# Performance work log

Hardware: AMD Instinct MI355X
Metric: run time of the kernel (lower is better)

The kernel has to match this reference:

```python
import jax, jax.numpy as jnp
import numpy as np

N = 8192
D = 512            # d_model
E = 8              # num_experts
H = 1024           # expert_hidden_dim
RH = 256           # router_hidden_dim
TOPK = 2
IN_DIM = 9 * D + 3
LN_EPS = 1e-5


def layernorm(x, g, b, eps=LN_EPS):
    m = jnp.mean(x, axis=-1, keepdims=True)
    v = jnp.mean((x - m) ** 2, axis=-1, keepdims=True)
    return (x - m) * jax.lax.rsqrt(v + eps) * g + b


def setup_inputs() -> dict:
    key = jax.random.key(0)
    ks = jax.random.split(key, 16)
    s_in = 1.0 / np.sqrt(IN_DIM)
    s_rh = 1.0 / np.sqrt(RH)
    s_h = 1.0 / np.sqrt(H)
    return {
        "z1": jax.random.normal(ks[0], (N, D), jnp.float32),
        "z2": jax.random.normal(ks[1], (N, D), jnp.float32),
        "z3": jax.random.normal(ks[2], (N, D), jnp.float32),
        "mask": jnp.ones((N, 3), jnp.float32),
        # LayerNorms
        "ln_g": jnp.ones((D,), jnp.float32), "ln_b": jnp.zeros((D,), jnp.float32),
        "lnp_g": jnp.ones((D,), jnp.float32), "lnp_b": jnp.zeros((D,), jnp.float32),
        "oln_g": jnp.ones((D,), jnp.float32), "oln_b": jnp.zeros((D,), jnp.float32),
        # Router MLP
        "r_w1": jax.random.normal(ks[3], (IN_DIM, RH), jnp.float32) * s_in,
        "r_b1": jnp.zeros((RH,), jnp.float32),
        "r_w2": jax.random.normal(ks[4], (RH, E), jnp.float32) * s_rh,
        "r_b2": jnp.zeros((E,), jnp.float32),
        "log_temp": jnp.array(np.log(1.0), jnp.float32),
        # Stacked experts: fc1 [E, IN_DIM, H], fc2 [E, H, D]
        "e_w1": jax.random.normal(ks[5], (E, IN_DIM, H), jnp.float32) * s_in,
        "e_b1": jnp.zeros((E, H), jnp.float32),
        "e_w2": jax.random.normal(ks[6], (E, H, D), jnp.float32) * s_h,
        "e_b2": jnp.zeros((E, D), jnp.float32),
    }


def reference(z1, z2, z3, mask, ln_g, ln_b, lnp_g, lnp_b, oln_g, oln_b,
              r_w1, r_b1, r_w2, r_b2, log_temp, e_w1, e_b1, e_w2, e_b2):
    # --- build fusion input ---
    z1n = layernorm(z1, ln_g, ln_b)
    z2n = layernorm(z2, ln_g, ln_b)
    z3n = layernorm(z3, ln_g, ln_b)
    d12 = layernorm(z1n - z2n, lnp_g, lnp_b)
    d13 = layernorm(z1n - z3n, lnp_g, lnp_b)
    d23 = layernorm(z2n - z3n, lnp_g, lnp_b)
    p12 = layernorm(z1n * z2n, lnp_g, lnp_b)
    p13 = layernorm(z1n * z3n, lnp_g, lnp_b)
    p23 = layernorm(z2n * z3n, lnp_g, lnp_b)
    x = jnp.concatenate([z1n, z2n, z3n, d12, d13, d23, p12, p13, p23, mask], axis=-1)  # [N, 9D+3]

    # --- router: MLP + temperature-scaled top-k softmax ---
    temp = jnp.clip(jnp.exp(log_temp), 1e-3, 100.0)
    rh = jax.nn.gelu(x @ r_w1 + r_b1, approximate=False)
    logits = (rh @ r_w2 + r_b2) / temp                      # [N, E]
    topv, topi = jax.lax.top_k(logits, TOPK)
    keep = jnp.zeros_like(logits).at[jnp.arange(logits.shape[0])[:, None], topi].set(1.0)
    masked_logits = jnp.where(keep == 0, -jnp.inf, logits)
    gate = jax.nn.softmax(masked_logits, axis=-1)           # [N, E]

    # --- dense expert compute (matches torch.stack over experts) ---
    eh = jax.nn.gelu(jnp.einsum('ni,eih->neh', x, e_w1) + e_b1, approximate=False)
    outs = jnp.einsum('neh,ehd->ned', eh, e_w2) + e_b2      # [N, E, D]
    z = jnp.einsum('ne,ned->nd', gate, outs)                # combine

    # --- masked residual ---
    denom = jnp.clip(jnp.sum(mask, axis=1, keepdims=True), 1.0, None)
    z_res = (mask[:, 0:1] * z1n + mask[:, 1:2] * z2n + mask[:, 2:3] * z3n) / denom
    z = z + z_res

    return layernorm(z, oln_g, oln_b)
```

## Files before the change

kernel.cpp:

```cpp
#include <hip/hip_runtime.h>
#include <math.h>

#define N_TOK 8192
#define DMODEL 512
#define NEXP 8
#define HEXP 1024
#define RHDIM 256
#define KP 4672
#define IN_REAL 4611
#define BK 64
#define NPAIR (N_TOK * 2)
#define MAXT 136

typedef unsigned short u16;
typedef __bf16 bf16x8 __attribute__((ext_vector_type(8)));
typedef float f32x4 __attribute__((ext_vector_type(4)));

__device__ inline u16 f2bf(float f) {
    union { float f; unsigned u; } x; x.f = f;
    unsigned r = x.u + 0x7FFFu + ((x.u >> 16) & 1u);
    return (u16)(r >> 16);
}
__device__ inline float bf2f(u16 u) {
    union { unsigned u; float f; } x; x.u = ((unsigned)u) << 16;
    return x.f;
}
__device__ inline float gelu_exact(float v) {
    return 0.5f * v * (1.f + erff(v * 0.70710678118654752440f));
}

__device__ inline void async_cp16(const u16* g, u16* l) {
    __builtin_amdgcn_global_load_lds(
        (const __attribute__((address_space(1))) unsigned int*)g,
        (__attribute__((address_space(3))) unsigned int*)l, 16, 0, 0);
}

template<int M>
__device__ inline void breduce(float (&v)[M], int tid, float* red) {
    #pragma unroll
    for (int o = 32; o > 0; o >>= 1)
        #pragma unroll
        for (int i = 0; i < M; i++) v[i] += __shfl_xor(v[i], o);
    __syncthreads();
    if ((tid & 63) == 0) {
        #pragma unroll
        for (int i = 0; i < M; i++) red[(tid >> 6) * M + i] = v[i];
    }
    __syncthreads();
    if (tid < M) {
        float S = 0.f;
        #pragma unroll
        for (int w8 = 0; w8 < 8; w8++) S += red[w8 * M + tid];
        red[96 + tid] = S;
    }
    __syncthreads();
    #pragma unroll
    for (int i = 0; i < M; i++) v[i] = red[96 + i];
}

__device__ inline float2 bstats512(float v, int tid, float* red) {
    float s = v, q = v * v;
    #pragma unroll
    for (int o = 32; o > 0; o >>= 1) {
        s += __shfl_xor(s, o);
        q += __shfl_xor(q, o);
    }
    __syncthreads();
    if ((tid & 63) == 0) { red[(tid >> 6) * 2] = s; red[(tid >> 6) * 2 + 1] = q; }
    __syncthreads();
    if (tid == 0) {
        float S = 0.f, Q = 0.f;
        #pragma unroll
        for (int i = 0; i < 8; i++) { S += red[i * 2]; Q += red[i * 2 + 1]; }
        float m = S * (1.f / 512.f);
        float var = fmaxf(Q * (1.f / 512.f) - m * m, 0.f);
        red[16] = m;
        red[17] = rsqrtf(var + 1e-5f);
    }
    __syncthreads();
    return make_float2(red[16], red[17]);
}

__global__ __launch_bounds__(256)
void transpose_f32_bf16(const float* __restrict__ src, u16* __restrict__ dhi, u16* __restrict__ dlo,
                        int K0, int KPd, int H, size_t sbatch, size_t dbatch) {
    __shared__ float tile[32][33];
    int bz = blockIdx.z;
    src += (size_t)bz * sbatch;
    size_t dob = (size_t)bz * dbatch;
    int k0 = blockIdx.x * 32, h0 = blockIdx.y * 32;
    int tx = threadIdx.x, ty = threadIdx.y;
    for (int i = ty; i < 32; i += 8) {
        int k = k0 + i;
        tile[i][tx] = (k < K0) ? src[(size_t)k * H + (h0 + tx)] : 0.f;
    }
    __syncthreads();
    for (int i = ty; i < 32; i += 8) {
        int h = h0 + i, k = k0 + tx;
        float v = tile[tx][i];
        u16 hv = f2bf(v);
        dhi[dob + (size_t)h * KPd + k] = hv;
        if (dlo) dlo[dob + (size_t)h * KPd + k] = f2bf(v - bf2f(hv));
    }
}

__global__ __launch_bounds__(512)
void build_x(const float* __restrict__ z1, const float* __restrict__ z2, const float* __restrict__ z3,
             const float* __restrict__ mask,
             const float* __restrict__ ln_g, const float* __restrict__ ln_b,
             const float* __restrict__ lnp_g, const float* __restrict__ lnp_b,
             u16* __restrict__ xhi, u16* __restrict__ xlo) {
    __shared__ float red[108];
    int n = blockIdx.x, d = threadIdx.x;
    float a = z1[(size_t)n * DMODEL + d];
    float b = z2[(size_t)n * DMODEL + d];
    float c = z3[(size_t)n * DMODEL + d];
    float gg = ln_g[d], bb = ln_b[d], pg = lnp_g[d], pb = lnp_b[d];
    size_t base = (size_t)n * KP;

    auto emit = [&](int seg, float v) {
        u16 h = f2bf(v);
        xhi[base + seg * DMODEL + d] = h;
        xlo[base + seg * DMODEL + d] = f2bf(v - bf2f(h));
    };
    auto lnv = [](float v, float s, float q, float g, float bo) {
        float m = s * (1.f / 512.f);
        float var = fmaxf(q * (1.f / 512.f) - m * m, 0.f);
        return (v - m) * rsqrtf(var + 1e-5f) * g + bo;
    };
    float v6[6] = {a, a * a, b, b * b, c, c * c};
    breduce<6>(v6, d, red);
    float z1n = lnv(a, v6[0], v6[1], gg, bb);
    float z2n = lnv(b, v6[2], v6[3], gg, bb);
    float z3n = lnv(c, v6[4], v6[5], gg, bb);
    emit(0, z1n); emit(1, z2n); emit(2, z3n);
    float d12 = z1n - z2n, d13 = z1n - z3n, d23 = z2n - z3n;
    float p12 = z1n * z2n, p13 = z1n * z3n, p23 = z2n * z3n;
    float v12[12] = {d12, d12 * d12, d13, d13 * d13, d23, d23 * d23,
                     p12, p12 * p12, p13, p13 * p13, p23, p23 * p23};
    breduce<12>(v12, d, red);
    emit(3, lnv(d12, v12[0], v12[1], pg, pb));
    emit(4, lnv(d13, v12[2], v12[3], pg, pb));
    emit(5, lnv(d23, v12[4], v12[5], pg, pb));
    emit(6, lnv(p12, v12[6], v12[7], pg, pb));
    emit(7, lnv(p13, v12[8], v12[9], pg, pb));
    emit(8, lnv(p23, v12[10], v12[11], pg, pb));
    if (d < 64) {
        int col = 9 * DMODEL + d;
        float v = (d < 3) ? mask[(size_t)n * 3 + d] : 0.f;
        u16 h = f2bf(v);
        xhi[base + col] = h;
        xlo[base + col] = f2bf(v - bf2f(h));
    }
}

#define GEMM_DEFS4                                                            \
    int t = threadIdx.x;                                                      \
    int lane = t & 63, w = t >> 6;                                            \
    int r8 = lane >> 3;                                                       \
    int ce = ((lane & 7) ^ r8) * 8;         \
    int fr = lane & 15, q4 = lane >> 4;                                       \
    int wm = (w & 1) * 64, wn = (w >> 1) * 64;                                \
    f32x4 acc[4][4];                                                          \
    { f32x4 z4 = {0.f, 0.f, 0.f, 0.f};                                        \
      _Pragma("unroll") for (int i = 0; i < 4; i++)                           \
      _Pragma("unroll") for (int j = 0; j < 4; j++) acc[i][j] = z4; }         \
    u16 *lAp[4], *lBp[4];                                                     \
    _Pragma("unroll") for (int i = 0; i < 4; i++) {                           \
        lAp[i] = lA + (w * 32 + 8 * i) * BK;                                  \
        lBp[i] = lB + (w * 32 + 8 * i) * BK;                                  \
    }

#define GEMM_KSTEP4                                                           \
        __syncthreads();                                                      \
        _Pragma("unroll") for (int i = 0; i < 4; i++) {                       \
            async_cp16(gA[i], lAp[i]); async_cp16(gB[i], lBp[i]);             \
            gA[i] += BK; gB[i] += BK;                                         \
        }                                                                     \
        __syncthreads();                                                      \
        _Pragma("unroll") for (int ks = 0; ks < 2; ks++) {                    \
            bf16x8 af[4], bfr[4];                                             \
            int cofs = (((q4 + ks * 4) ^ (fr & 7)) * 8);                      \
            _Pragma("unroll") for (int i = 0; i < 4; i++)                     \
                af[i] = *(const bf16x8*)&lA[(wm + i * 16 + fr) * BK + cofs];  \
            _Pragma("unroll") for (int j = 0; j < 4; j++)                     \
                bfr[j] = *(const bf16x8*)&lB[(wn + j * 16 + fr) * BK + cofs]; \
            _Pragma("unroll") for (int i = 0; i < 4; i++)                     \
            _Pragma("unroll") for (int j = 0; j < 4; j++)                     \
                acc[i][j] = __builtin_amdgcn_mfma_f32_16x16x32_bf16(af[i], bfr[j], acc[i][j], 0, 0, 0); \
        }

#define GEMM_DEFS8                                                            \
    int t = threadIdx.x;                                                      \
    int lane = t & 63, w = t >> 6;                                            \
    int r8 = lane >> 3;                                                       \
    int ce = ((lane & 7) ^ r8) * 8;         \
    int fr = lane & 15, q4 = lane >> 4;                                       \
    int wm = (w & 1) * 64, wn = (w >> 1) * 64;                                \
    f32x4 acc[4][4];                                                          \
    { f32x4 z4 = {0.f, 0.f, 0.f, 0.f};                                        \
      _Pragma("unroll") for (int i = 0; i < 4; i++)                           \
      _Pragma("unroll") for (int j = 0; j < 4; j++) acc[i][j] = z4; }         \
    u16 *lAp[2], *lBp[4];                                                     \
    _Pragma("unroll") for (int i = 0; i < 2; i++)                             \
        lAp[i] = lA + (w * 16 + 8 * i) * BK;                                  \
    _Pragma("unroll") for (int i = 0; i < 4; i++)                             \
        lBp[i] = lB + (w * 32 + 8 * i) * BK;

#define GEMM_KSTEP8                                                           \
        __syncthreads();                                                      \
        _Pragma("unroll") for (int i = 0; i < 2; i++) {                       \
            async_cp16(gA[i], lAp[i]); gA[i] += BK;                           \
        }                                                                     \
        _Pragma("unroll") for (int i = 0; i < 4; i++) {                       \
            async_cp16(gB[i], lBp[i]); gB[i] += BK;                           \
        }                                                                     \
        __syncthreads();                                                      \
        _Pragma("unroll") for (int ks = 0; ks < 2; ks++) {                    \
            bf16x8 af[4], bfr[4];                                             \
            int cofs = (((q4 + ks * 4) ^ (fr & 7)) * 8);                      \
            _Pragma("unroll") for (int i = 0; i < 4; i++)                     \
                af[i] = *(const bf16x8*)&lA[(wm + i * 16 + fr) * BK + cofs];  \
            _Pragma("unroll") for (int j = 0; j < 4; j++)                     \
                bfr[j] = *(const bf16x8*)&lB[(wn + j * 16 + fr) * BK + cofs]; \
            _Pragma("unroll") for (int i = 0; i < 4; i++)                     \
            _Pragma("unroll") for (int j = 0; j < 4; j++)                     \
                acc[i][j] = __builtin_amdgcn_mfma_f32_16x16x32_bf16(af[i], bfr[j], acc[i][j], 0, 0, 0); \
        }

__global__ __launch_bounds__(512, 4)
void router_fc1(const u16* __restrict__ xhi, const u16* __restrict__ xlo,
                const u16* __restrict__ rw1hi, const u16* __restrict__ rw1lo,
                float* __restrict__ rpart) {
    int mt = blockIdx.x & 63, part = blockIdx.x >> 6;
    int region = part >> 1, half = part & 1;
    const u16* A = (region == 2) ? xlo : xhi;
    const u16* B = (region == 1) ? rw1lo : rw1hi;
    int kbase = half ? 2304 : 0;
    int klen  = half ? 2368 : 2304;

    __shared__ u16 lA[128 * BK];
    __shared__ u16 lB[256 * BK];
    GEMM_DEFS8

    const u16* gA[2]; const u16* gB[4];
    #pragma unroll
    for (int i = 0; i < 2; i++)
        gA[i] = A + (size_t)(mt * 128 + w * 16 + 8 * i + r8) * KP + kbase + ce;
    #pragma unroll
    for (int i = 0; i < 4; i++)
        gB[i] = B + (size_t)(w * 32 + 8 * i + r8) * KP + kbase + ce;

    for (int k0 = 0; k0 < klen; k0 += BK) {
        GEMM_KSTEP8
    }
    float* outp = rpart + (size_t)part * ((size_t)N_TOK * RHDIM);
    int cn = lane & 15;
    #pragma unroll
    for (int i = 0; i < 4; i++)
        #pragma unroll
        for (int rr = 0; rr < 4; rr++) {
            int mg = mt * 128 + wm + i * 16 + q4 * 4 + rr;
            #pragma unroll
            for (int j = 0; j < 4; j++)
                outp[(size_t)mg * RHDIM + wn + j * 16 + cn] = acc[i][j][rr];
        }
}

__global__ __launch_bounds__(256)
void logits_topk(const float* __restrict__ rpart, const float* __restrict__ r_b1,
                 const float* __restrict__ r_w2, const float* __restrict__ r_b2,
                 const float* __restrict__ log_temp,
                 float* __restrict__ pgate, int* __restrict__ pexp,
                 int* __restrict__ lists, int* __restrict__ counts) {
    int t = threadIdx.x, wave = t >> 6, lane = t & 63;
    int n = blockIdx.x * 4 + wave;
    float4 v = {0.f, 0.f, 0.f, 0.f};
    #pragma unroll
    for (int p = 0; p < 6; p++) {
        float4 s = ((const float4*)(rpart + (size_t)p * ((size_t)N_TOK * RHDIM) + (size_t)n * RHDIM))[lane];
        v.x += s.x; v.y += s.y; v.z += s.z; v.w += s.w;
    }
    float4 b1 = ((const float4*)r_b1)[lane];
    float rh0 = gelu_exact(v.x + b1.x);
    float rh1 = gelu_exact(v.y + b1.y);
    float rh2 = gelu_exact(v.z + b1.z);
    float rh3 = gelu_exact(v.w + b1.w);
    int k = lane * 4;
    float p8[8];
    #pragma unroll
    for (int e = 0; e < 8; e++)
        p8[e] = rh0 * r_w2[(k + 0) * 8 + e] + rh1 * r_w2[(k + 1) * 8 + e]
              + rh2 * r_w2[(k + 2) * 8 + e] + rh3 * r_w2[(k + 3) * 8 + e];
    #pragma unroll
    for (int o = 32; o > 0; o >>= 1)
        #pragma unroll
        for (int e = 0; e < 8; e++) p8[e] += __shfl_xor(p8[e], o);
    if (lane == 0) {
        float temp = fminf(fmaxf(expf(log_temp[0]), 1e-3f), 100.f);
        float l[8];
        #pragma unroll
        for (int e = 0; e < 8; e++) l[e] = (p8[e] + r_b2[e]) / temp;
        int i1 = 0;
        #pragma unroll
        for (int i = 1; i < 8; i++) if (l[i] > l[i1]) i1 = i;
        int i2 = (i1 == 0) ? 1 : 0;
        #pragma unroll
        for (int i = 0; i < 8; i++) if (i != i1 && l[i] > l[i2]) i2 = i;
        float p = expf(l[i2] - l[i1]);
        float g1 = 1.f / (1.f + p);
        float g2 = p / (1.f + p);
        pgate[n * 2] = g1;     pexp[n * 2] = i1;
        pgate[n * 2 + 1] = g2; pexp[n * 2 + 1] = i2;
        int pos1 = atomicAdd(&counts[i1], 1);
        lists[(size_t)i1 * N_TOK + pos1] = n * 2;
        int pos2 = atomicAdd(&counts[i2], 1);
        lists[(size_t)i2 * N_TOK + pos2] = n * 2 + 1;
    }
}

__global__ void sched_tiles(const int* __restrict__ counts, int* __restrict__ tiles) {
    if (threadIdx.x == 0) {
        int tcount = 0;
        for (int e = 0; e < NEXP; e++) {
            int nt = (counts[e] + 127) >> 7;
            for (int mt = 0; mt < nt; mt++) tiles[tcount++] = (e << 16) | mt;
        }
        for (; tcount < MAXT; tcount++) tiles[tcount] = -1;
    }
}

__global__ __launch_bounds__(256, 4)
void expert_fc1(const u16* __restrict__ xhi, const u16* __restrict__ w1t,
                const float* __restrict__ e_b1, const int* __restrict__ lists,
                const int* __restrict__ counts, const int* __restrict__ tiles,
                u16* __restrict__ eh) {
    int nt = blockIdx.x & 7, ti = blockIdx.x >> 3;
    int info = tiles[ti];
    if (info < 0) return;
    int e = info >> 16, mt = info & 0xFFFF;
    int cnt = counts[e];

    __shared__ u16 lA[128 * BK];
    __shared__ u16 lB[128 * BK];
    __shared__ int rows[128];
    int tt = threadIdx.x;
    if (tt < 128) {
        int m = mt * 128 + tt;
        rows[tt] = lists[(size_t)e * N_TOK + (m < cnt ? m : 0)];
    }
    __syncthreads();

    GEMM_DEFS4

    const u16* wb = w1t + (size_t)e * HEXP * KP + (size_t)(nt * 128) * KP;
    const u16* gA[4]; const u16* gB[4];
    #pragma unroll
    for (int i = 0; i < 4; i++) {
        gA[i] = xhi + (size_t)(rows[w * 32 + 8 * i + r8] >> 1) * KP + ce;
        gB[i] = wb + (size_t)(w * 32 + 8 * i + r8) * KP + ce;
    }

    for (int k0 = 0; k0 < KP; k0 += BK) {
        GEMM_KSTEP4
    }
    int cn = lane & 15;
    #pragma unroll
    for (int i = 0; i < 4; i++)
        #pragma unroll
        for (int rr = 0; rr < 4; rr++) {
            int ml = wm + i * 16 + q4 * 4 + rr;
            int mg = mt * 128 + ml;
            if (mg < cnt) {
                int entry = rows[ml];
                #pragma unroll
                for (int j = 0; j < 4; j++) {
                    int col = nt * 128 + wn + j * 16 + cn;
                    float v = acc[i][j][rr] + e_b1[(size_t)e * HEXP + col];
                    eh[(size_t)entry * HEXP + col] = f2bf(gelu_exact(v));
                }
            }
        }
}

__global__ __launch_bounds__(512, 4)
void expert_fc2(const u16* __restrict__ eh, const u16* __restrict__ w2t,
                const int* __restrict__ lists, const int* __restrict__ counts,
                const int* __restrict__ tiles, float* __restrict__ outs) {
    int nt = blockIdx.x & 1, ti = blockIdx.x >> 1;
    int info = tiles[ti];
    if (info < 0) return;
    int e = info >> 16, mt = info & 0xFFFF;
    int cnt = counts[e];

    __shared__ u16 lA[128 * BK];
    __shared__ u16 lB[256 * BK];
    __shared__ int rows[128];
    int tt = threadIdx.x;
    if (tt < 128) {
        int m = mt * 128 + tt;
        rows[tt] = lists[(size_t)e * N_TOK + (m < cnt ? m : 0)];
    }
    __syncthreads();

    GEMM_DEFS8

    const u16* wb = w2t + (size_t)e * DMODEL * HEXP + (size_t)(nt * 256) * HEXP;
    const u16* gA[2]; const u16* gB[4];
    #pragma unroll
    for (int i = 0; i < 2; i++)
        gA[i] = eh + (size_t)rows[w * 16 + 8 * i + r8] * HEXP + ce;
    #pragma unroll
    for (int i = 0; i < 4; i++)
        gB[i] = wb + (size_t)(w * 32 + 8 * i + r8) * HEXP + ce;

    for (int k0 = 0; k0 < HEXP; k0 += BK) {
        GEMM_KSTEP8
    }
    int cn = lane & 15;
    #pragma unroll
    for (int i = 0; i < 4; i++)
        #pragma unroll
        for (int rr = 0; rr < 4; rr++) {
            int ml = wm + i * 16 + q4 * 4 + rr;
            int mg = mt * 128 + ml;
            if (mg < cnt) {
                int entry = rows[ml];
                #pragma unroll
                for (int j = 0; j < 4; j++) {
                    int col = nt * 256 + wn + j * 16 + cn;
                    outs[(size_t)entry * DMODEL + col] = acc[i][j][rr];
                }
            }
        }
}

__global__ __launch_bounds__(512)
void combine_ln(const float* __restrict__ outs, const float* __restrict__ pgate,
                const int* __restrict__ pexp, const float* __restrict__ e_b2,
                const float* __restrict__ mask, const u16* __restrict__ xhi,
                const u16* __restrict__ xlo, const float* __restrict__ oln_g,
                const float* __restrict__ oln_b, float* __restrict__ out) {
    __shared__ float red[18];
    int n = blockIdx.x, d = threadIdx.x;
    float g0 = pgate[n * 2], g1 = pgate[n * 2 + 1];
    int e0 = pexp[n * 2], e1 = pexp[n * 2 + 1];
    float o = g0 * (outs[(size_t)(n * 2) * DMODEL + d] + e_b2[(size_t)e0 * DMODEL + d])
            + g1 * (outs[(size_t)(n * 2 + 1) * DMODEL + d] + e_b2[(size_t)e1 * DMODEL + d]);
    float m0 = mask[n * 3 + 0], m1 = mask[n * 3 + 1], m2 = mask[n * 3 + 2];
    float denom = fmaxf(m0 + m1 + m2, 1.f);
    size_t xb = (size_t)n * KP;
    float z1n = bf2f(xhi[xb + d]) + bf2f(xlo[xb + d]);
    float z2n = bf2f(xhi[xb + DMODEL + d]) + bf2f(xlo[xb + DMODEL + d]);
    float z3n = bf2f(xhi[xb + 2 * DMODEL + d]) + bf2f(xlo[xb + 2 * DMODEL + d]);
    float z = o + (m0 * z1n + m1 * z2n + m2 * z3n) / denom;
    float2 st = bstats512(z, d, red);
    out[(size_t)n * DMODEL + d] = (z - st.x) * st.y * oln_g[d] + oln_b[d];
}

extern "C" void kernel_launch(void* const* d_in, const int* in_sizes, int n_in,
                              void* d_out, int out_size, void* d_ws, size_t ws_size,
                              hipStream_t stream) {
    (void)in_sizes; (void)n_in; (void)out_size; (void)ws_size;
    const float* z1       = (const float*)d_in[0];
    const float* z2       = (const float*)d_in[1];
    const float* z3       = (const float*)d_in[2];
    const float* mask     = (const float*)d_in[3];
    const float* ln_g     = (const float*)d_in[4];
    const float* ln_b     = (const float*)d_in[5];
    const float* lnp_g    = (const float*)d_in[6];
    const float* lnp_b    = (const float*)d_in[7];
    const float* oln_g    = (const float*)d_in[8];
    const float* oln_b    = (const float*)d_in[9];
    const float* r_w1     = (const float*)d_in[10];
    const float* r_b1     = (const float*)d_in[11];
    const float* r_w2     = (const float*)d_in[12];
    const float* r_b2     = (const float*)d_in[13];
    const float* log_temp = (const float*)d_in[14];
    const float* e_w1     = (const float*)d_in[15];
    const float* e_b1     = (const float*)d_in[16];
    const float* e_w2     = (const float*)d_in[17];
    const float* e_b2     = (const float*)d_in[18];
    float* out = (float*)d_out;

    char* p = (char*)d_ws;
    auto carve = [&](size_t bytes) { char* r = p; p += (bytes + 255) & ~(size_t)255; return r; };
    u16*   xhi    = (u16*)carve((size_t)N_TOK * KP * 2);
    u16*   xlo    = (u16*)carve((size_t)N_TOK * KP * 2);
    u16*   w1t    = (u16*)carve((size_t)NEXP * HEXP * KP * 2);
    u16*   w2t    = (u16*)carve((size_t)NEXP * DMODEL * HEXP * 2);
    u16*   rw1hi  = (u16*)carve((size_t)RHDIM * KP * 2);
    u16*   rw1lo  = (u16*)carve((size_t)RHDIM * KP * 2);
    float* rpart  = (float*)carve((size_t)6 * N_TOK * RHDIM * 4);
    u16*   eh     = (u16*)carve((size_t)NPAIR * HEXP * 2);
    float* outsb  = (float*)carve((size_t)NPAIR * DMODEL * 4);
    float* pgate  = (float*)carve((size_t)NPAIR * 4);
    int*   pexp   = (int*)carve((size_t)NPAIR * 4);
    int*   lists  = (int*)carve((size_t)NEXP * N_TOK * 4);
    int*   counts = (int*)carve(256);
    int*   tiles  = (int*)carve(MAXT * 4);

    dim3 tb(32, 8);
    transpose_f32_bf16<<<dim3(KP / 32, HEXP / 32, NEXP), tb, 0, stream>>>(
        e_w1, w1t, (u16*)nullptr, IN_REAL, KP, HEXP, (size_t)IN_REAL * HEXP, (size_t)HEXP * KP);
    transpose_f32_bf16<<<dim3(HEXP / 32, DMODEL / 32, NEXP), tb, 0, stream>>>(
        e_w2, w2t, (u16*)nullptr, HEXP, HEXP, DMODEL, (size_t)HEXP * DMODEL, (size_t)DMODEL * HEXP);
    transpose_f32_bf16<<<dim3(KP / 32, RHDIM / 32, 1), tb, 0, stream>>>(
        r_w1, rw1hi, rw1lo, IN_REAL, KP, RHDIM, (size_t)0, (size_t)0);

    build_x<<<N_TOK, 512, 0, stream>>>(z1, z2, z3, mask, ln_g, ln_b, lnp_g, lnp_b, xhi, xlo);

    router_fc1<<<384, 512, 0, stream>>>(xhi, xlo, rw1hi, rw1lo, rpart);

    hipMemsetAsync(counts, 0, 256, stream);
    logits_topk<<<N_TOK / 4, 256, 0, stream>>>(rpart, r_b1, r_w2, r_b2, log_temp,
                                               pgate, pexp, lists, counts);
    sched_tiles<<<1, 64, 0, stream>>>(counts, tiles);

    expert_fc1<<<MAXT * 8, 256, 0, stream>>>(xhi, w1t, e_b1, lists, counts, tiles, eh);
    expert_fc2<<<MAXT * 2, 512, 0, stream>>>(eh, w2t, lists, counts, tiles, outsb);

    combine_ln<<<N_TOK, 512, 0, stream>>>(outsb, pgate, pexp, e_b2, mask, xhi, xlo, oln_g, oln_b, out);
}
```

Measured before the change: 978.0 us.

## Vectorize elementwise kernels, shrink block sizes, and split router hi*hi K range

build_x and combine_ln now use 128 threads per token, with each thread handling 4 elements through float4/ushort4 loads and stores. The block reduction is simplified to two wavefronts. The transpose kernel writes 4-wide packed bf16 stores. router_fc1 splits the dominant hi*hi product into four K chunks, giving 512 blocks and 8 partial buffers, to raise parallelism at the cost of more partial-sum traffic in logits_topk.

```diff
diff --git a/kernel.cpp b/kernel.cpp
--- a/kernel.cpp
+++ b/kernel.cpp
@@ -11,6 +11,7 @@
 #define BK 64
 #define NPAIR (N_TOK * 2)
 #define MAXT 136
+#define NRPART 8
 
 typedef unsigned short u16;
 typedef __bf16 bf16x8 __attribute__((ext_vector_type(8)));
@@ -36,49 +37,19 @@
 }
 
 template<int M>
-__device__ inline void breduce(float (&v)[M], int tid, float* red) {
+__device__ inline void bred128(float (&v)[M], int t, float* red) {
     #pragma unroll
     for (int o = 32; o > 0; o >>= 1)
         #pragma unroll
         for (int i = 0; i < M; i++) v[i] += __shfl_xor(v[i], o);
     __syncthreads();
-    if ((tid & 63) == 0) {
-        #pragma unroll
-        for (int i = 0; i < M; i++) red[(tid >> 6) * M + i] = v[i];
+    if ((t & 63) == 0) {
+        #pragma unroll
+        for (int i = 0; i < M; i++) red[(t >> 6) * M + i] = v[i];
     }
     __syncthreads();
-    if (tid < M) {
-        float S = 0.f;
-        #pragma unroll
-        for (int w8 = 0; w8 < 8; w8++) S += red[w8 * M + tid];
-        red[96 + tid] = S;
-    }
-    __syncthreads();
-    #pragma unroll
-    for (int i = 0; i < M; i++) v[i] = red[96 + i];
-}
-
-__device__ inline float2 bstats512(float v, int tid, float* red) {
-    float s = v, q = v * v;
-    #pragma unroll
-    for (int o = 32; o > 0; o >>= 1) {
-        s += __shfl_xor(s, o);
-        q += __shfl_xor(q, o);
-    }
-    __syncthreads();
-    if ((tid & 63) == 0) { red[(tid >> 6) * 2] = s; red[(tid >> 6) * 2 + 1] = q; }
-    __syncthreads();
-    if (tid == 0) {
-        float S = 0.f, Q = 0.f;
-        #pragma unroll
-        for (int i = 0; i < 8; i++) { S += red[i * 2]; Q += red[i * 2 + 1]; }
-        float m = S * (1.f / 512.f);
-        float var = fmaxf(Q * (1.f / 512.f) - m * m, 0.f);
-        red[16] = m;
-        red[17] = rsqrtf(var + 1e-5f);
-    }
-    __syncthreads();
-    return make_float2(red[16], red[17]);
+    #pragma unroll
+    for (int i = 0; i < M; i++) v[i] = red[i] + red[M + i];
 }
 
 __global__ __launch_bounds__(256)
@@ -95,62 +66,110 @@
         tile[i][tx] = (k < K0) ? src[(size_t)k * H + (h0 + tx)] : 0.f;
     }
     __syncthreads();
-    for (int i = ty; i < 32; i += 8) {
-        int h = h0 + i, k = k0 + tx;
-        float v = tile[tx][i];
-        u16 hv = f2bf(v);
-        dhi[dob + (size_t)h * KPd + k] = hv;
-        if (dlo) dlo[dob + (size_t)h * KPd + k] = f2bf(v - bf2f(hv));
-    }
-}
-
-__global__ __launch_bounds__(512)
+    int tid = ty * 32 + tx;
+    int h = tid >> 3, kq = tid & 7;
+    int hg = h0 + h, kg = k0 + kq * 4;
+    ushort4 hv, lv;
+    float v0 = tile[kq * 4 + 0][h], v1 = tile[kq * 4 + 1][h];
+    float v2 = tile[kq * 4 + 2][h], v3 = tile[kq * 4 + 3][h];
+    hv.x = f2bf(v0); hv.y = f2bf(v1); hv.z = f2bf(v2); hv.w = f2bf(v3);
+    *(ushort4*)(dhi + dob + (size_t)hg * KPd + kg) = hv;
+    if (dlo) {
+        lv.x = f2bf(v0 - bf2f(hv.x)); lv.y = f2bf(v1 - bf2f(hv.y));
+        lv.z = f2bf(v2 - bf2f(hv.z)); lv.w = f2bf(v3 - bf2f(hv.w));
+        *(ushort4*)(dlo + dob + (size_t)hg * KPd + kg) = lv;
+    }
+}
+
+__global__ __launch_bounds__(128)
 void build_x(const float* __restrict__ z1, const float* __restrict__ z2, const float* __restrict__ z3,
              const float* __restrict__ mask,
              const float* __restrict__ ln_g, const float* __restrict__ ln_b,
              const float* __restrict__ lnp_g, const float* __restrict__ lnp_b,
              u16* __restrict__ xhi, u16* __restrict__ xlo) {
-    __shared__ float red[108];
-    int n = blockIdx.x, d = threadIdx.x;
-    float a = z1[(size_t)n * DMODEL + d];
-    float b = z2[(size_t)n * DMODEL + d];
-    float c = z3[(size_t)n * DMODEL + d];
-    float gg = ln_g[d], bb = ln_b[d], pg = lnp_g[d], pb = lnp_b[d];
+    __shared__ float red[24];
+    int n = blockIdx.x, t = threadIdx.x;
+    int d0 = t * 4;
+    float4 a4 = ((const float4*)(z1 + (size_t)n * DMODEL))[t];
+    float4 b4 = ((const float4*)(z2 + (size_t)n * DMODEL))[t];
+    float4 c4 = ((const float4*)(z3 + (size_t)n * DMODEL))[t];
+    float a[4] = {a4.x, a4.y, a4.z, a4.w};
+    float b[4] = {b4.x, b4.y, b4.z, b4.w};
+    float c[4] = {c4.x, c4.y, c4.z, c4.w};
+    float4 gg4 = ((const float4*)ln_g)[t], bb4 = ((const float4*)ln_b)[t];
+    float4 pg4 = ((const float4*)lnp_g)[t], pb4 = ((const float4*)lnp_b)[t];
+    float gg[4] = {gg4.x, gg4.y, gg4.z, gg4.w}, bb[4] = {bb4.x, bb4.y, bb4.z, bb4.w};
+    float pg[4] = {pg4.x, pg4.y, pg4.z, pg4.w}, pb[4] = {pb4.x, pb4.y, pb4.z, pb4.w};
     size_t base = (size_t)n * KP;
 
-    auto emit = [&](int seg, float v) {
-        u16 h = f2bf(v);
-        xhi[base + seg * DMODEL + d] = h;
-        xlo[base + seg * DMODEL + d] = f2bf(v - bf2f(h));
+    auto emit = [&](int seg, const float* v) {
+        ushort4 hv, lv;
+        hv.x = f2bf(v[0]); hv.y = f2bf(v[1]); hv.z = f2bf(v[2]); hv.w = f2bf(v[3]);
+        lv.x = f2bf(v[0] - bf2f(hv.x)); lv.y = f2bf(v[1] - bf2f(hv.y));
+        lv.z = f2bf(v[2] - bf2f(hv.z)); lv.w = f2bf(v[3] - bf2f(hv.w));
+        *(ushort4*)(xhi + base + seg * DMODEL + d0) = hv;
+        *(ushort4*)(xlo + base + seg * DMODEL + d0) = lv;
     };
-    auto lnv = [](float v, float s, float q, float g, float bo) {
-        float m = s * (1.f / 512.f);
-        float var = fmaxf(q * (1.f / 512.f) - m * m, 0.f);
-        return (v - m) * rsqrtf(var + 1e-5f) * g + bo;
+    float v6[6] = {0.f, 0.f, 0.f, 0.f, 0.f, 0.f};
+    #pragma unroll
+    for (int j = 0; j < 4; j++) {
+        v6[0] += a[j]; v6[1] += a[j] * a[j];
+        v6[2] += b[j]; v6[3] += b[j] * b[j];
+        v6[4] += c[j]; v6[5] += c[j] * c[j];
+    }
+    bred128<6>(v6, t, red);
+    auto lnstats = [](float s, float q, float* m, float* r) {
+        *m = s * (1.f / 512.f);
+        float var = fmaxf(q * (1.f / 512.f) - (*m) * (*m), 0.f);
+        *r = rsqrtf(var + 1e-5f);
     };
-    float v6[6] = {a, a * a, b, b * b, c, c * c};
-    breduce<6>(v6, d, red);
-    float z1n = lnv(a, v6[0], v6[1], gg, bb);
-    float z2n = lnv(b, v6[2], v6[3], gg, bb);
-    float z3n = lnv(c, v6[4], v6[5], gg, bb);
-    emit(0, z1n); emit(1, z2n); emit(2, z3n);
-    float d12 = z1n - z2n, d13 = z1n - z3n, d23 = z2n - z3n;
-    float p12 = z1n * z2n, p13 = z1n * z3n, p23 = z2n * z3n;
-    float v12[12] = {d12, d12 * d12, d13, d13 * d13, d23, d23 * d23,
-                     p12, p12 * p12, p13, p13 * p13, p23, p23 * p23};
-    breduce<12>(v12, d, red);
-    emit(3, lnv(d12, v12[0], v12[1], pg, pb));
-    emit(4, lnv(d13, v12[2], v12[3], pg, pb));
-    emit(5, lnv(d23, v12[4], v12[5], pg, pb));
-    emit(6, lnv(p12, v12[6], v12[7], pg, pb));
-    emit(7, lnv(p13, v12[8], v12[9], pg, pb));
-    emit(8, lnv(p23, v12[10], v12[11], pg, pb));
-    if (d < 64) {
-        int col = 9 * DMODEL + d;
-        float v = (d < 3) ? mask[(size_t)n * 3 + d] : 0.f;
-        u16 h = f2bf(v);
-        xhi[base + col] = h;
-        xlo[base + col] = f2bf(v - bf2f(h));
+    float m1, r1, m2, r2, m3, r3;
+    lnstats(v6[0], v6[1], &m1, &r1);
+    lnstats(v6[2], v6[3], &m2, &r2);
+    lnstats(v6[4], v6[5], &m3, &r3);
+    float za[4], zb[4], zc[4];
+    #pragma unroll
+    for (int j = 0; j < 4; j++) {
+        za[j] = (a[j] - m1) * r1 * gg[j] + bb[j];
+        zb[j] = (b[j] - m2) * r2 * gg[j] + bb[j];
+        zc[j] = (c[j] - m3) * r3 * gg[j] + bb[j];
+    }
+    emit(0, za); emit(1, zb); emit(2, zc);
+    float d12[4], d13[4], d23[4], p12[4], p13[4], p23[4];
+    float v12[12];
+    #pragma unroll
+    for (int i = 0; i < 12; i++) v12[i] = 0.f;
+    #pragma unroll
+    for (int j = 0; j < 4; j++) {
+        d12[j] = za[j] - zb[j]; d13[j] = za[j] - zc[j]; d23[j] = zb[j] - zc[j];
+        p12[j] = za[j] * zb[j]; p13[j] = za[j] * zc[j]; p23[j] = zb[j] * zc[j];
+        v12[0] += d12[j]; v12[1] += d12[j] * d12[j];
+        v12[2] += d13[j]; v12[3] += d13[j] * d13[j];
+        v12[4] += d23[j]; v12[5] += d23[j] * d23[j];
+        v12[6] += p12[j]; v12[7] += p12[j] * p12[j];
+        v12[8] += p13[j]; v12[9] += p13[j] * p13[j];
+        v12[10] += p23[j]; v12[11] += p23[j] * p23[j];
+    }
+    bred128<12>(v12, t, red);
+    float* segs[6] = {d12, d13, d23, p12, p13, p23};
+    #pragma unroll
+    for (int s = 0; s < 6; s++) {
+        float ms, rs;
+        lnstats(v12[s * 2], v12[s * 2 + 1], &ms, &rs);
+        float v[4];
+        #pragma unroll
+        for (int j = 0; j < 4; j++) v[j] = (segs[s][j] - ms) * rs * pg[j] + pb[j];
+        emit(3 + s, v);
+    }
+    if (t < 16) {
+        float v[4] = {0.f, 0.f, 0.f, 0.f};
+        if (t == 0) { v[0] = mask[(size_t)n * 3]; v[1] = mask[(size_t)n * 3 + 1]; v[2] = mask[(size_t)n * 3 + 2]; }
+        ushort4 hv, lv;
+        hv.x = f2bf(v[0]); hv.y = f2bf(v[1]); hv.z = f2bf(v[2]); hv.w = f2bf(v[3]);
+        lv.x = f2bf(v[0] - bf2f(hv.x)); lv.y = f2bf(v[1] - bf2f(hv.y));
+        lv.z = f2bf(v[2] - bf2f(hv.z)); lv.w = f2bf(v[3] - bf2f(hv.w));
+        *(ushort4*)(xhi + base + 9 * DMODEL + t * 4) = hv;
+        *(ushort4*)(xlo + base + 9 * DMODEL + t * 4) = lv;
     }
 }
 
@@ -233,11 +252,19 @@
                 const u16* __restrict__ rw1hi, const u16* __restrict__ rw1lo,
                 float* __restrict__ rpart) {
     int mt = blockIdx.x & 63, part = blockIdx.x >> 6;
-    int region = part >> 1, half = part & 1;
-    const u16* A = (region == 2) ? xlo : xhi;
-    const u16* B = (region == 1) ? rw1lo : rw1hi;
-    int kbase = half ? 2304 : 0;
-    int klen  = half ? 2368 : 2304;
+    const u16* A; const u16* B;
+    int kbase, klen;
+    if (part < 4) {
+        A = xhi; B = rw1hi;
+        kbase = part * 1152;
+        klen = (part == 3) ? 1216 : 1152;
+    } else {
+        int half = part & 1;
+        kbase = half ? 2304 : 0;
+        klen  = half ? 2368 : 2304;
+        if (part < 6) { A = xhi; B = rw1lo; }
+        else          { A = xlo; B = rw1hi; }
+    }
 
     __shared__ u16 lA[128 * BK];
     __shared__ u16 lB[256 * BK];
@@ -277,7 +304,7 @@
     int n = blockIdx.x * 4 + wave;
     float4 v = {0.f, 0.f, 0.f, 0.f};
     #pragma unroll
-    for (int p = 0; p < 6; p++) {
+    for (int p = 0; p < NRPART; p++) {
         float4 s = ((const float4*)(rpart + (size_t)p * ((size_t)N_TOK * RHDIM) + (size_t)n * RHDIM))[lane];
         v.x += s.x; v.y += s.y; v.z += s.z; v.w += s.w;
     }
@@ -435,27 +462,63 @@
         }
 }
 
-__global__ __launch_bounds__(512)
+__global__ __launch_bounds__(128)
 void combine_ln(const float* __restrict__ outs, const float* __restrict__ pgate,
                 const int* __restrict__ pexp, const float* __restrict__ e_b2,
                 const float* __restrict__ mask, const u16* __restrict__ xhi,
                 const u16* __restrict__ xlo, const float* __restrict__ oln_g,
                 const float* __restrict__ oln_b, float* __restrict__ out) {
-    __shared__ float red[18];
-    int n = blockIdx.x, d = threadIdx.x;
+    __shared__ float red[4];
+    int n = blockIdx.x, t = threadIdx.x;
     float g0 = pgate[n * 2], g1 = pgate[n * 2 + 1];
     int e0 = pexp[n * 2], e1 = pexp[n * 2 + 1];
-    float o = g0 * (outs[(size_t)(n * 2) * DMODEL + d] + e_b2[(size_t)e0 * DMODEL + d])
-            + g1 * (outs[(size_t)(n * 2 + 1) * DMODEL + d] + e_b2[(size_t)e1 * DMODEL + d]);
+    float4 o0 = ((const float4*)(outs + (size_t)(n * 2) * DMODEL))[t];
+    float4 o1 = ((const float4*)(outs + (size_t)(n * 2 + 1) * DMODEL))[t];
+    float4 b0 = ((const float4*)(e_b2 + (size_t)e0 * DMODEL))[t];
+    float4 b1 = ((const float4*)(e_b2 + (size_t)e1 * DMODEL))[t];
+    float o[4] = {g0 * (o0.x + b0.x) + g1 * (o1.x + b1.x),
+                  g0 * (o0.y + b0.y) + g1 * (o1.y + b1.y),
+                  g0 * (o0.z + b0.z) + g1 * (o1.z + b1.z),
+                  g0 * (o0.w + b0.w) + g1 * (o1.w + b1.w)};
     float m0 = mask[n * 3 + 0], m1 = mask[n * 3 + 1], m2 = mask[n * 3 + 2];
     float denom = fmaxf(m0 + m1 + m2, 1.f);
     size_t xb = (size_t)n * KP;
-    float z1n = bf2f(xhi[xb + d]) + bf2f(xlo[xb + d]);
-    float z2n = bf2f(xhi[xb + DMODEL + d]) + bf2f(xlo[xb + DMODEL + d]);
-    float z3n = bf2f(xhi[xb + 2 * DMODEL + d]) + bf2f(xlo[xb + 2 * DMODEL + d]);
-    float z = o + (m0 * z1n + m1 * z2n + m2 * z3n) / denom;
-    float2 st = bstats512(z, d, red);
-    out[(size_t)n * DMODEL + d] = (z - st.x) * st.y * oln_g[d] + oln_b[d];
+    ushort4 h1 = *(const ushort4*)(xhi + xb + t * 4);
+    ushort4 l1 = *(const ushort4*)(xlo + xb + t * 4);
+    ushort4 h2 = *(const ushort4*)(xhi + xb + DMODEL + t * 4);
+    ushort4 l2 = *(const ushort4*)(xlo + xb + DMODEL + t * 4);
+    ushort4 h3 = *(const ushort4*)(xhi + xb + 2 * DMODEL + t * 4);
+    ushort4 l3 = *(const ushort4*)(xlo + xb + 2 * DMODEL + t * 4);
+    float z[4], s = 0.f, q = 0.f;
+    u16 h1a[4] = {h1.x, h1.y, h1.z, h1.w}, l1a[4] = {l1.x, l1.y, l1.z, l1.w};
+    u16 h2a[4] = {h2.x, h2.y, h2.z, h2.w}, l2a[4] = {l2.x, l2.y, l2.z, l2.w};
+    u16 h3a[4] = {h3.x, h3.y, h3.z, h3.w}, l3a[4] = {l3.x, l3.y, l3.z, l3.w};
+    #pragma unroll
+    for (int j = 0; j < 4; j++) {
+        float z1n = bf2f(h1a[j]) + bf2f(l1a[j]);
+        float z2n = bf2f(h2a[j]) + bf2f(l2a[j]);
+        float z3n = bf2f(h3a[j]) + bf2f(l3a[j]);
+        z[j] = o[j] + (m0 * z1n + m1 * z2n + m2 * z3n) / denom;
+        s += z[j]; q += z[j] * z[j];
+    }
+    #pragma unroll
+    for (int ofs = 32; ofs > 0; ofs >>= 1) {
+        s += __shfl_xor(s, ofs);
+        q += __shfl_xor(q, ofs);
+    }
+    if ((t & 63) == 0) { red[(t >> 6) * 2] = s; red[(t >> 6) * 2 + 1] = q; }
+    __syncthreads();
+    s = red[0] + red[2]; q = red[1] + red[3];
+    float m = s * (1.f / 512.f);
+    float var = fmaxf(q * (1.f / 512.f) - m * m, 0.f);
+    float r = rsqrtf(var + 1e-5f);
+    float4 g4 = ((const float4*)oln_g)[t], be4 = ((const float4*)oln_b)[t];
+    float4 res;
+    res.x = (z[0] - m) * r * g4.x + be4.x;
+    res.y = (z[1] - m) * r * g4.y + be4.y;
+    res.z = (z[2] - m) * r * g4.z + be4.z;
+    res.w = (z[3] - m) * r * g4.w + be4.w;
+    ((float4*)(out + (size_t)n * DMODEL))[t] = res;
 }
 
 extern "C" void kernel_launch(void* const* d_in, const int* in_sizes, int n_in,
@@ -491,7 +554,7 @@
     u16*   w2t    = (u16*)carve((size_t)NEXP * DMODEL * HEXP * 2);
     u16*   rw1hi  = (u16*)carve((size_t)RHDIM * KP * 2);
     u16*   rw1lo  = (u16*)carve((size_t)RHDIM * KP * 2);
-    float* rpart  = (float*)carve((size_t)6 * N_TOK * RHDIM * 4);
+    float* rpart  = (float*)carve((size_t)NRPART * N_TOK * RHDIM * 4);
     u16*   eh     = (u16*)carve((size_t)NPAIR * HEXP * 2);
     float* outsb  = (float*)carve((size_t)NPAIR * DMODEL * 4);
     float* pgate  = (float*)carve((size_t)NPAIR * 4);
@@ -508,9 +571,9 @@
     transpose_f32_bf16<<<dim3(KP / 32, RHDIM / 32, 1), tb, 0, stream>>>(
         r_w1, rw1hi, rw1lo, IN_REAL, KP, RHDIM, (size_t)0, (size_t)0);
 
-    build_x<<<N_TOK, 512, 0, stream>>>(z1, z2, z3, mask, ln_g, ln_b, lnp_g, lnp_b, xhi, xlo);
-
-    router_fc1<<<384, 512, 0, stream>>>(xhi, xlo, rw1hi, rw1lo, rpart);
+    build_x<<<N_TOK, 128, 0, stream>>>(z1, z2, z3, mask, ln_g, ln_b, lnp_g, lnp_b, xhi, xlo);
+
+    router_fc1<<<512, 512, 0, stream>>>(xhi, xlo, rw1hi, rw1lo, rpart);
 
     hipMemsetAsync(counts, 0, 256, stream);
     logits_topk<<<N_TOK / 4, 256, 0, stream>>>(rpart, r_b1, r_w2, r_b2, log_temp,
@@ -520,5 +583,5 @@
     expert_fc1<<<MAXT * 8, 256, 0, stream>>>(xhi, w1t, e_b1, lists, counts, tiles, eh);
     expert_fc2<<<MAXT * 2, 512, 0, stream>>>(eh, w2t, lists, counts, tiles, outsb);
 
-    combine_ln<<<N_TOK, 512, 0, stream>>>(outsb, pgate, pexp, e_b2, mask, xhi, xlo, oln_g, oln_b, out);
-}
+    combine_ln<<<N_TOK, 128, 0, stream>>>(outsb, pgate, pexp, e_b2, mask, xhi, xlo, oln_g, oln_b, out);
+}
```

Measured after the change: 923.5 us. 5.6% less time.
